# Performance work log

Hardware: AMD Instinct MI355X
Metric: run time of the kernel (lower is better)

Reference implementation:

```python
import jax, jax.numpy as jnp
import numpy as np

N_HEAD = 8
D_HEAD = 64
HIDDEN = 512
T = 2048
BS = 4
SCALE = D_HEAD ** -0.5


def setup_inputs() -> dict:
    key = jax.random.key(0)
    k1, k2, k3 = jax.random.split(key, 3)
    x = jax.random.normal(k1, (BS, T, HIDDEN), dtype=jnp.float32)
    # torch Linear weight is (out,in); we store as (in,out) for x @ W
    W_qkv = jax.random.normal(k2, (HIDDEN, (2 * N_HEAD + 1) * D_HEAD), dtype=jnp.float32) * 0.02
    W_out = jax.random.normal(k3, (D_HEAD, HIDDEN), dtype=jnp.float32) * 0.02
    return {"x": x, "W_qkv": W_qkv, "W_out": W_out}


def reference(x, W_qkv, W_out):
    bs, t, h = x.shape
    qkv = x @ W_qkv  # (bs, t, (2H+1)*d)
    q, k, v = jnp.split(qkv, [N_HEAD * D_HEAD, 2 * N_HEAD * D_HEAD], axis=-1)
    q = q.reshape(bs, t, N_HEAD, D_HEAD)
    k = k.reshape(bs, t, N_HEAD, D_HEAD)
    # v is shared across heads: (bs, t, d)
    score = jnp.einsum("bqhd,bkhd->bhqk", q, k) * SCALE
    causal = jnp.triu(jnp.full((t, t), -jnp.inf, dtype=score.dtype), 1)
    score = score + causal[None, None, :, :]
    prob = jax.nn.softmax(score, axis=-1)  # (bs, H, t, t)
    attn_vec = jnp.einsum("bhqk,bkd->bhqd", prob, v)  # shared V broadcast over heads
    m_attn_vec = jnp.mean(attn_vec, axis=1)  # head-mean: (bs, t, d)
    out = m_attn_vec @ W_out  # (bs, t, hidden)
    return out, attn_vec
```

## Files before the change

kernel.cpp:

```cpp
#include <hip/hip_runtime.h>
#include <hip/hip_bf16.h>

#define NHEAD  8
#define DHEAD  64
#define HIDDEN 512
#define SEQ_T  2048
#define BATCH  4
#define NQKV   1088
#define NT     32
#define NROWS  (BATCH * SEQ_T)
#define NBH    (BATCH * NHEAD)
#define QSC    (0.125f * 1.44269504f)

typedef __attribute__((ext_vector_type(8))) short short8;
typedef __attribute__((ext_vector_type(4))) float f32x4;

__device__ __forceinline__ unsigned short f2bf(float f) {
  unsigned int u = __float_as_uint(f);
  u += 0x7FFFu + ((u >> 16) & 1u);
  return (unsigned short)(u >> 16);
}

__device__ __forceinline__ void load_lds16(const unsigned short* g, unsigned short* l) {
  __builtin_amdgcn_global_load_lds((const __attribute__((address_space(1))) void*)g,
                                   (__attribute__((address_space(3))) void*)l, 16, 0, 0);
}

#define DPPF(x, ctrl) \
  __int_as_float(__builtin_amdgcn_update_dpp(0, __float_as_int(x), (ctrl), 0xF, 0xF, true))
__device__ __forceinline__ float rsum16(float x) {
  x += DPPF(x, 0xB1);
  x += DPPF(x, 0x4E);
  x += DPPF(x, 0x141);
  x += DPPF(x, 0x140);
  return x;
}

__global__ __launch_bounds__(256) void cvt_x(const float* __restrict__ x,
                                             unsigned short* __restrict__ xb) {
  const size_t i0 = ((size_t)blockIdx.x * 256 + threadIdx.x) * 8;
  float4 a = *(const float4*)(x + i0);
  float4 b = *(const float4*)(x + i0 + 4);
  ushort4 u0, u1;
  u0.x = f2bf(a.x); u0.y = f2bf(a.y); u0.z = f2bf(a.z); u0.w = f2bf(a.w);
  u1.x = f2bf(b.x); u1.y = f2bf(b.y); u1.z = f2bf(b.z); u1.w = f2bf(b.w);
  *(ushort4*)(xb + i0) = u0;
  *(ushort4*)(xb + i0 + 4) = u1;
}

__global__ __launch_bounds__(256) void wt_bf16(const float* __restrict__ W,
                                               unsigned short* __restrict__ Wt) {
  const int n0 = blockIdx.x * 64;
  const int k0 = blockIdx.y * 64;
  const int tid = threadIdx.x;
  __shared__ float T[64 * 65];

#pragma unroll
  for (int i = 0; i < 4; ++i) {
    int f = tid + i * 256;
    int r = f >> 4;
    int c4 = (f & 15) * 4;
    float4 v = *(const float4*)(W + (size_t)(k0 + r) * NQKV + n0 + c4);
    T[r * 65 + c4 + 0] = v.x;
    T[r * 65 + c4 + 1] = v.y;
    T[r * 65 + c4 + 2] = v.z;
    T[r * 65 + c4 + 3] = v.w;
  }
  __syncthreads();

#pragma unroll
  for (int i = 0; i < 4; ++i) {
    int f = tid + i * 256;
    int n = f >> 4;
    int k4 = (f & 15) * 4;
    ushort4 u;
    u.x = f2bf(T[(k4 + 0) * 65 + n]);
    u.y = f2bf(T[(k4 + 1) * 65 + n]);
    u.z = f2bf(T[(k4 + 2) * 65 + n]);
    u.w = f2bf(T[(k4 + 3) * 65 + n]);
    *(ushort4*)(Wt + (size_t)(n0 + n) * HIDDEN + k0 + k4) = u;
  }
}

__global__ __launch_bounds__(256) void qkv_mfma(const unsigned short* __restrict__ Xb,
                                                const unsigned short* __restrict__ Wt,
                                                unsigned short* __restrict__ Y) {
  __shared__ __align__(16) unsigned short As[128 * 64];
  __shared__ __align__(16) unsigned short Bs[64 * 64];
  const int L = blockIdx.x;
  const int slot = L >> 3;
  const int bm = (L & 7) * 8 + (slot & 7);
  const int bn = slot >> 3;
  const int tid = threadIdx.x;
  const int wave = tid >> 6;
  const int lane = tid & 63;
  const int quad = lane >> 4;
  const int l15 = lane & 15;
  const int lrow = lane >> 3;
  const int lchunk = lane & 7;

  const unsigned short* xrow = Xb + (size_t)bm * 128 * HIDDEN;
  const unsigned short* wrow = Wt + (size_t)bn * 64 * HIDDEN;

  f32x4 acc[2][4];
#pragma unroll
  for (int mt = 0; mt < 2; ++mt)
#pragma unroll
    for (int nt = 0; nt < 4; ++nt) acc[mt][nt] = (f32x4){0.f, 0.f, 0.f, 0.f};

  for (int k0 = 0; k0 < HIDDEN; k0 += 64) {
    __syncthreads();
#pragma unroll
    for (int c = 0; c < 4; ++c) {
      int call = wave * 4 + c;
      int m = call * 8 + lrow;
      int clog = lchunk ^ lrow;
      load_lds16(xrow + (size_t)m * HIDDEN + k0 + clog * 8, &As[call * 512]);
    }
#pragma unroll
    for (int c = 0; c < 2; ++c) {
      int call = wave * 2 + c;
      int n = call * 8 + lrow;
      int clog = lchunk ^ lrow;
      load_lds16(wrow + (size_t)n * HIDDEN + k0 + clog * 8, &Bs[call * 512]);
    }
    __syncthreads();

#pragma unroll
    for (int ks = 0; ks < 2; ++ks) {
      short8 a[2], b[4];
#pragma unroll
      for (int mt = 0; mt < 2; ++mt) {
        int m = wave * 32 + mt * 16 + l15;
        int phys = (ks * 4 + quad) ^ (l15 & 7);
        a[mt] = *(const short8*)&As[m * 64 + phys * 8];
      }
#pragma unroll
      for (int nt = 0; nt < 4; ++nt) {
        int n = nt * 16 + l15;
        int phys = (ks * 4 + quad) ^ (l15 & 7);
        b[nt] = *(const short8*)&Bs[n * 64 + phys * 8];
      }
#pragma unroll
      for (int mt = 0; mt < 2; ++mt)
#pragma unroll
        for (int nt = 0; nt < 4; ++nt)
          acc[mt][nt] = __builtin_amdgcn_mfma_f32_16x16x32_bf16(a[mt], b[nt], acc[mt][nt], 0, 0, 0);
    }
  }

  const float qs = (bn < 8) ? QSC : 1.0f;
#pragma unroll
  for (int mt = 0; mt < 2; ++mt)
#pragma unroll
    for (int r = 0; r < 4; ++r) {
      int row = bm * 128 + wave * 32 + mt * 16 + quad * 4 + r;
#pragma unroll
      for (int nt = 0; nt < 4; ++nt) {
        int col = bn * 64 + nt * 16 + l15;
        Y[(size_t)row * NQKV + col] = f2bf(acc[mt][nt][r] * qs);
      }
    }
}

__global__ __launch_bounds__(256) void v_transpose(const unsigned short* __restrict__ qkv,
                                                   unsigned short* __restrict__ vt) {
  const int b = blockIdx.x >> 5;
  const int k0 = (blockIdx.x & 31) * 64;
  const int tid = threadIdx.x;
  __shared__ unsigned short Vs[64 * 66];

#pragma unroll
  for (int i = 0; i < 8; ++i) {
    int c = tid + i * 256;
    int row = c >> 5;
    int col2 = c & 31;
    unsigned int v = *(const unsigned int*)(qkv + (size_t)(b * SEQ_T + k0 + row) * NQKV + 1024 + col2 * 2);
    *(unsigned int*)&Vs[row * 66 + col2 * 2] = v;
  }
  __syncthreads();

#pragma unroll
  for (int i = 0; i < 16; ++i) {
    int f = tid + i * 256;
    int d = f >> 6;
    int n = f & 63;
    int c = ((n & 3) << 4) | (n >> 2);
    vt[((size_t)b * DHEAD + d) * SEQ_T + k0 + n] = Vs[c * 66 + d];
  }
}

__global__ __launch_bounds__(256, 4) void attn_pass(const unsigned short* __restrict__ qkv,
                                                    const unsigned short* __restrict__ vt,
                                                    float* __restrict__ part0,
                                                    unsigned short* __restrict__ pbuf,
                                                    float* __restrict__ lbuf) {
  const int bh = blockIdx.x;
  const int y = blockIdx.y;
  const int qt = 15 - (y >> 1);
  const int kh = y & 1;
  const int b = bh >> 3;
  const int h = bh & 7;
  const int tid = threadIdx.x;
  const int wave = tid >> 6;
  const int lane = tid & 63;
  const int quad = lane >> 4;
  const int l15 = lane & 15;

  __shared__ __align__(16) unsigned short Ks[64 * 64];
  __shared__ __align__(16) unsigned short Vts[64 * 64];
  __shared__ __align__(16) unsigned short Ps[128 * 72];

  const unsigned short* bq = qkv + (size_t)b * SEQ_T * NQKV;
  const unsigned short* bvt = vt + (size_t)b * DHEAD * SEQ_T;

  const int q0 = qt * 128;
  const int kbeg = kh ? (qt + 1) : 0;
  const int kend = kh ? (2 * qt + 1) : qt;

  short8 aq[2][2];
#pragma unroll
  for (int s = 0; s < 2; ++s) {
    const unsigned short* qp = bq + (size_t)(q0 + s * 64 + wave * 16 + l15) * NQKV + h * 64 + quad * 8;
    aq[s][0] = *(const short8*)qp;
    aq[s][1] = *(const short8*)(qp + 32);
  }

  f32x4 o[2][4];
#pragma unroll
  for (int s = 0; s < 2; ++s)
#pragma unroll
    for (int t = 0; t < 4; ++t) o[s][t] = (f32x4){0.f, 0.f, 0.f, 0.f};
  float l_part[2][4] = {{0.f, 0.f, 0.f, 0.f}, {0.f, 0.f, 0.f, 0.f}};

  const int srow = tid >> 3;
  const int sch = (tid & 7) ^ (srow & 7);
  const int ph0 = (quad ^ (l15 & 7)) * 8;

  for (int kt = kbeg; kt <= kend; ++kt) {
    const int k0 = kt * 64;
    __syncthreads();
#pragma unroll
    for (int c = 0; c < 2; ++c) {
      load_lds16(bq + (size_t)(k0 + c * 32 + srow) * NQKV + 512 + h * 64 + sch * 8,
                 &Ks[c * 2048 + wave * 512]);
      load_lds16(bvt + (size_t)(c * 32 + srow) * SEQ_T + k0 + sch * 8,
                 &Vts[c * 2048 + wave * 512]);
    }
    __syncthreads();

    const bool needMask = (k0 + 63) > q0;

    short8 bk[4][2];
#pragma unroll
    for (int t = 0; t < 4; ++t) {
      const unsigned short* kp = &Ks[(l15 + 16 * t) * 64];
      bk[t][0] = *(const short8*)(kp + ph0);
      bk[t][1] = *(const short8*)(kp + (ph0 ^ 32));
    }

#pragma unroll
    for (int s = 0; s < 2; ++s) {
      f32x4 pr[4];
#pragma unroll
      for (int t = 0; t < 4; ++t) {
        f32x4 sv = (f32x4){0.f, 0.f, 0.f, 0.f};
        sv = __builtin_amdgcn_mfma_f32_16x16x32_bf16(aq[s][0], bk[t][0], sv, 0, 0, 0);
        sv = __builtin_amdgcn_mfma_f32_16x16x32_bf16(aq[s][1], bk[t][1], sv, 0, 0, 0);
        pr[t] = sv;
      }
      const int rbase = s * 64 + wave * 16 + quad * 4;
#pragma unroll
      for (int t = 0; t < 4; ++t)
#pragma unroll
        for (int r = 0; r < 4; ++r) {
          float p = __builtin_amdgcn_exp2f(pr[t][r]);
          if (needMask)
            p = (k0 + 16 * t + l15 <= q0 + rbase + r) ? p : 0.f;
          l_part[s][r] += p;
          pr[t][r] = p;
        }
#pragma unroll
      for (int r = 0; r < 4; ++r) {
        uint2 w;
        w.x = __builtin_amdgcn_perm(__float_as_uint(pr[1][r]), __float_as_uint(pr[0][r]), 0x07060302u);
        w.y = __builtin_amdgcn_perm(__float_as_uint(pr[3][r]), __float_as_uint(pr[2][r]), 0x07060302u);
        *(uint2*)&Ps[(rbase + r) * 72 + 4 * l15] = w;
      }
    }

    short8 bv[4][2];
#pragma unroll
    for (int t = 0; t < 4; ++t) {
      const unsigned short* vp = &Vts[(l15 + 16 * t) * 64];
      bv[t][0] = *(const short8*)(vp + ph0);
      bv[t][1] = *(const short8*)(vp + (ph0 ^ 32));
    }
    short8 ap[2][2];
#pragma unroll
    for (int s = 0; s < 2; ++s) {
      const unsigned short* pp = &Ps[(s * 64 + wave * 16 + l15) * 72];
      ap[s][0] = *(const short8*)(pp + quad * 8);
      ap[s][1] = *(const short8*)(pp + 32 + quad * 8);
    }

#pragma unroll
    for (int t = 0; t < 4; ++t)
#pragma unroll
      for (int s = 0; s < 2; ++s) {
        o[s][t] = __builtin_amdgcn_mfma_f32_16x16x32_bf16(ap[s][0], bv[t][0], o[s][t], 0, 0, 0);
        o[s][t] = __builtin_amdgcn_mfma_f32_16x16x32_bf16(ap[s][1], bv[t][1], o[s][t], 0, 0, 0);
      }
  }

#pragma unroll
  for (int s = 0; s < 2; ++s) {
#pragma unroll
    for (int r = 0; r < 4; ++r) {
      float l = rsum16(l_part[s][r]);
      const int trow = q0 + s * 64 + wave * 16 + quad * 4 + r;
      if (l15 == 0) lbuf[kh * (NBH * SEQ_T) + bh * SEQ_T + trow] = l;
      const size_t base = ((size_t)bh * SEQ_T + trow) * DHEAD;
      if (kh == 0) {
#pragma unroll
        for (int t = 0; t < 4; ++t) part0[base + l15 + 16 * t] = o[s][t][r];
      } else {
#pragma unroll
        for (int t = 0; t < 4; ++t) pbuf[base + l15 + 16 * t] = f2bf(o[s][t][r]);
      }
    }
  }
}

__global__ __launch_bounds__(256) void merge_attn(float* __restrict__ attnv,
                                                  const unsigned short* __restrict__ pbuf,
                                                  const float* __restrict__ lbuf) {
  const int tid = threadIdx.x;
  const int row = blockIdx.x * 16 + (tid >> 4);
  const int d4 = (tid & 15) * 4;
  const float inv = 1.0f / (lbuf[row] + lbuf[NBH * SEQ_T + row]);
  const size_t idx = (size_t)row * DHEAD + d4;
  float4 A = *(const float4*)(attnv + idx);
  ushort4 B = *(const ushort4*)(pbuf + idx);
  float4 o;
  o.x = (A.x + __uint_as_float((unsigned int)B.x << 16)) * inv;
  o.y = (A.y + __uint_as_float((unsigned int)B.y << 16)) * inv;
  o.z = (A.z + __uint_as_float((unsigned int)B.z << 16)) * inv;
  o.w = (A.w + __uint_as_float((unsigned int)B.w << 16)) * inv;
  *(float4*)(attnv + idx) = o;
}

__global__ __launch_bounds__(256) void out_gemm(const float* __restrict__ attn,
                                                const float* __restrict__ Wout,
                                                float* __restrict__ out) {
  const int row0 = blockIdx.x * 16;
  const int tid = threadIdx.x;
  __shared__ float Ms[16][64];

#pragma unroll
  for (int i = 0; i < 4; ++i) {
    int f = tid + i * 256;
    int lr = f >> 6;
    int d = f & 63;
    int row = row0 + lr;
    int b = row >> 11;
    int t = row & 2047;
    float sum = 0.f;
#pragma unroll
    for (int hh = 0; hh < NHEAD; ++hh) {
      sum += attn[((size_t)(b * NHEAD + hh) * SEQ_T + t) * DHEAD + d];
    }
    Ms[lr][d] = sum * (1.0f / NHEAD);
  }
  __syncthreads();

  const int c0 = tid * 2;
  float a0[16], a1[16];
#pragma unroll
  for (int i = 0; i < 16; ++i) { a0[i] = 0.f; a1[i] = 0.f; }

  for (int d = 0; d < 64; ++d) {
    float2 w = *(const float2*)(Wout + (size_t)d * HIDDEN + c0);
#pragma unroll
    for (int lr = 0; lr < 16; ++lr) {
      float m = Ms[lr][d];
      a0[lr] += m * w.x;
      a1[lr] += m * w.y;
    }
  }
#pragma unroll
  for (int lr = 0; lr < 16; ++lr) {
    float2 v = make_float2(a0[lr], a1[lr]);
    *(float2*)(out + (size_t)(row0 + lr) * HIDDEN + c0) = v;
  }
}

extern "C" void kernel_launch(void* const* d_in, const int* in_sizes, int n_in,
                              void* d_out, int out_size, void* d_ws, size_t ws_size,
                              hipStream_t stream) {
  const float* x     = (const float*)d_in[0];
  const float* W_qkv = (const float*)d_in[1];
  const float* W_out = (const float*)d_in[2];

  float* out      = (float*)d_out;
  float* attn_vec = out + (size_t)BATCH * SEQ_T * HIDDEN;

  unsigned short* qkv = (unsigned short*)d_ws;
  unsigned short* vt  = qkv + (size_t)NROWS * NQKV;
  unsigned short* xb  = vt + (size_t)BATCH * DHEAD * SEQ_T;
  unsigned short* Wt  = xb + (size_t)NROWS * HIDDEN;
  unsigned short* pbuf = xb;
  float*          lbuf = (float*)Wt;

  cvt_x<<<dim3(NROWS * HIDDEN / (256 * 8)), 256, 0, stream>>>(x, xb);
  wt_bf16<<<dim3(17, 8), 256, 0, stream>>>(W_qkv, Wt);
  qkv_mfma<<<dim3(64 * 17), 256, 0, stream>>>(xb, Wt, qkv);
  v_transpose<<<dim3(BATCH * NT), 256, 0, stream>>>(qkv, vt);
  attn_pass<<<dim3(NBH, 32), 256, 0, stream>>>(qkv, vt, attn_vec, pbuf, lbuf);
  merge_attn<<<dim3(NBH * SEQ_T / 16), 256, 0, stream>>>(attn_vec, pbuf, lbuf);
  out_gemm<<<dim3(512), 256, 0, stream>>>(attn_vec, W_out, out);
}
```

Baseline: 155.4 us.

## Fuse prep kernels, merge split-K into out GEMM, register-prefetch K/V tiles

Combines the x conversion and W transpose into one launch, folds the split-K attention merge into the output projection kernel, and replaces direct global-to-LDS loads in the attention loop with register-staged prefetch of the next K/V tile. The fusions remove two kernel launches and one full read/write pass over attn_vec. The register prefetch aims to overlap global loads with compute, at the cost of extra VGPRs and explicit LDS stores. Because the merge now reads part0 and writes attnv through the same buffer, each element is read and then written by the same thread, which is safe.

```diff
diff --git a/kernel.cpp b/kernel.cpp
--- a/kernel.cpp
+++ b/kernel.cpp
@@ -36,25 +36,27 @@
   return x;
 }
 
-__global__ __launch_bounds__(256) void cvt_x(const float* __restrict__ x,
-                                             unsigned short* __restrict__ xb) {
-  const size_t i0 = ((size_t)blockIdx.x * 256 + threadIdx.x) * 8;
-  float4 a = *(const float4*)(x + i0);
-  float4 b = *(const float4*)(x + i0 + 4);
-  ushort4 u0, u1;
-  u0.x = f2bf(a.x); u0.y = f2bf(a.y); u0.z = f2bf(a.z); u0.w = f2bf(a.w);
-  u1.x = f2bf(b.x); u1.y = f2bf(b.y); u1.z = f2bf(b.z); u1.w = f2bf(b.w);
-  *(ushort4*)(xb + i0) = u0;
-  *(ushort4*)(xb + i0 + 4) = u1;
-}
-
-__global__ __launch_bounds__(256) void wt_bf16(const float* __restrict__ W,
-                                               unsigned short* __restrict__ Wt) {
-  const int n0 = blockIdx.x * 64;
-  const int k0 = blockIdx.y * 64;
+__global__ __launch_bounds__(256) void prep(const float* __restrict__ x,
+                                            const float* __restrict__ W,
+                                            unsigned short* __restrict__ xb,
+                                            unsigned short* __restrict__ Wt) {
+  const int bx = blockIdx.x;
   const int tid = threadIdx.x;
+  if (bx < 2048) {
+    const size_t i0 = ((size_t)bx * 256 + tid) * 8;
+    float4 a = *(const float4*)(x + i0);
+    float4 b = *(const float4*)(x + i0 + 4);
+    ushort4 u0, u1;
+    u0.x = f2bf(a.x); u0.y = f2bf(a.y); u0.z = f2bf(a.z); u0.w = f2bf(a.w);
+    u1.x = f2bf(b.x); u1.y = f2bf(b.y); u1.z = f2bf(b.z); u1.w = f2bf(b.w);
+    *(ushort4*)(xb + i0) = u0;
+    *(ushort4*)(xb + i0 + 4) = u1;
+    return;
+  }
+  const int idx = bx - 2048;
+  const int n0 = (idx % 17) * 64;
+  const int k0 = (idx / 17) * 64;
   __shared__ float T[64 * 65];
-
 #pragma unroll
   for (int i = 0; i < 4; ++i) {
     int f = tid + i * 256;
@@ -67,7 +69,6 @@
     T[r * 65 + c4 + 3] = v.w;
   }
   __syncthreads();
-
 #pragma unroll
   for (int i = 0; i < 4; ++i) {
     int f = tid + i * 256;
@@ -236,16 +237,30 @@
   const int srow = tid >> 3;
   const int sch = (tid & 7) ^ (srow & 7);
   const int ph0 = (quad ^ (l15 & 7)) * 8;
+  const int lslot = wave * 512 + lane * 8;
+
+  uint4 kpref[2], vpref[2];
+#pragma unroll
+  for (int c = 0; c < 2; ++c) {
+    kpref[c] = *(const uint4*)(bq + (size_t)(kbeg * 64 + c * 32 + srow) * NQKV + 512 + h * 64 + sch * 8);
+    vpref[c] = *(const uint4*)(bvt + (size_t)(c * 32 + srow) * SEQ_T + kbeg * 64 + sch * 8);
+  }
 
   for (int kt = kbeg; kt <= kend; ++kt) {
     const int k0 = kt * 64;
     __syncthreads();
 #pragma unroll
     for (int c = 0; c < 2; ++c) {
-      load_lds16(bq + (size_t)(k0 + c * 32 + srow) * NQKV + 512 + h * 64 + sch * 8,
-                 &Ks[c * 2048 + wave * 512]);
-      load_lds16(bvt + (size_t)(c * 32 + srow) * SEQ_T + k0 + sch * 8,
-                 &Vts[c * 2048 + wave * 512]);
+      *(uint4*)&Ks[c * 2048 + lslot] = kpref[c];
+      *(uint4*)&Vts[c * 2048 + lslot] = vpref[c];
+    }
+    if (kt < kend) {
+      const int kn = (kt + 1) * 64;
+#pragma unroll
+      for (int c = 0; c < 2; ++c) {
+        kpref[c] = *(const uint4*)(bq + (size_t)(kn + c * 32 + srow) * NQKV + 512 + h * 64 + sch * 8);
+        vpref[c] = *(const uint4*)(bvt + (size_t)(c * 32 + srow) * SEQ_T + kn + sch * 8);
+      }
     }
     __syncthreads();
 
@@ -332,27 +347,12 @@
   }
 }
 
-__global__ __launch_bounds__(256) void merge_attn(float* __restrict__ attnv,
-                                                  const unsigned short* __restrict__ pbuf,
-                                                  const float* __restrict__ lbuf) {
-  const int tid = threadIdx.x;
-  const int row = blockIdx.x * 16 + (tid >> 4);
-  const int d4 = (tid & 15) * 4;
-  const float inv = 1.0f / (lbuf[row] + lbuf[NBH * SEQ_T + row]);
-  const size_t idx = (size_t)row * DHEAD + d4;
-  float4 A = *(const float4*)(attnv + idx);
-  ushort4 B = *(const ushort4*)(pbuf + idx);
-  float4 o;
-  o.x = (A.x + __uint_as_float((unsigned int)B.x << 16)) * inv;
-  o.y = (A.y + __uint_as_float((unsigned int)B.y << 16)) * inv;
-  o.z = (A.z + __uint_as_float((unsigned int)B.z << 16)) * inv;
-  o.w = (A.w + __uint_as_float((unsigned int)B.w << 16)) * inv;
-  *(float4*)(attnv + idx) = o;
-}
-
-__global__ __launch_bounds__(256) void out_gemm(const float* __restrict__ attn,
-                                                const float* __restrict__ Wout,
-                                                float* __restrict__ out) {
+__global__ __launch_bounds__(256) void out_merge(const float* __restrict__ part0,
+                                                 const unsigned short* __restrict__ pbuf,
+                                                 const float* __restrict__ lbuf,
+                                                 const float* __restrict__ Wout,
+                                                 float* __restrict__ attnv,
+                                                 float* __restrict__ out) {
   const int row0 = blockIdx.x * 16;
   const int tid = threadIdx.x;
   __shared__ float Ms[16][64];
@@ -368,7 +368,12 @@
     float sum = 0.f;
 #pragma unroll
     for (int hh = 0; hh < NHEAD; ++hh) {
-      sum += attn[((size_t)(b * NHEAD + hh) * SEQ_T + t) * DHEAD + d];
+      size_t ridx = (size_t)(b * NHEAD + hh) * SEQ_T + t;
+      float inv = 1.0f / (lbuf[ridx] + lbuf[NBH * SEQ_T + ridx]);
+      size_t idx = ridx * DHEAD + d;
+      float m = (part0[idx] + __uint_as_float((unsigned int)pbuf[idx] << 16)) * inv;
+      attnv[idx] = m;
+      sum += m;
     }
     Ms[lr][d] = sum * (1.0f / NHEAD);
   }
@@ -412,11 +417,9 @@
   unsigned short* pbuf = xb;
   float*          lbuf = (float*)Wt;
 
-  cvt_x<<<dim3(NROWS * HIDDEN / (256 * 8)), 256, 0, stream>>>(x, xb);
-  wt_bf16<<<dim3(17, 8), 256, 0, stream>>>(W_qkv, Wt);
+  prep<<<dim3(2048 + 136), 256, 0, stream>>>(x, W_qkv, xb, Wt);
   qkv_mfma<<<dim3(64 * 17), 256, 0, stream>>>(xb, Wt, qkv);
   v_transpose<<<dim3(BATCH * NT), 256, 0, stream>>>(qkv, vt);
   attn_pass<<<dim3(NBH, 32), 256, 0, stream>>>(qkv, vt, attn_vec, pbuf, lbuf);
-  merge_attn<<<dim3(NBH * SEQ_T / 16), 256, 0, stream>>>(attn_vec, pbuf, lbuf);
-  out_gemm<<<dim3(512), 256, 0, stream>>>(attn_vec, W_out, out);
-}
+  out_merge<<<dim3(512), 256, 0, stream>>>(attn_vec, pbuf, lbuf, W_out, attn_vec, out);
+}
```

Result: slower. 199.6 us (+28.5%).
